# Performance work log

Hardware: AMD Instinct MI355X
Metric: run time of the kernel (lower is better)

Reference implementation:

```python
import jax, jax.numpy as jnp
import numpy as np

N = 100000          # total nodes
G = 128             # number of graphs
D_IN, D_H, D_OUT = 512, 1024, 512
E = 1600000         # edges (unused by the math, matches forward signature)


def setup_inputs() -> dict:
    key = jax.random.key(0)
    ks = jax.random.split(key, 9)
    x = jax.random.normal(ks[0], (N, D_IN), dtype=jnp.float32)
    edge_index = jax.random.randint(ks[1], (2, E), 0, N, dtype=jnp.int64)
    # sorted batch ids; guarantee every graph id appears at least once
    batch = jnp.sort(jnp.concatenate([
        jnp.arange(G, dtype=jnp.int64),
        jax.random.randint(ks[2], (N - G,), 0, G, dtype=jnp.int64),
    ]))
    s = 0.02
    W0 = jax.random.normal(ks[3], (D_IN, D_H), dtype=jnp.float32) * s
    b0 = jnp.zeros((D_H,), dtype=jnp.float32)
    W1 = jax.random.normal(ks[4], (D_H, D_H), dtype=jnp.float32) * s
    b1 = jnp.zeros((D_H,), dtype=jnp.float32)
    W2 = jax.random.normal(ks[5], (D_H, D_OUT), dtype=jnp.float32) * s
    b2 = jnp.zeros((D_OUT,), dtype=jnp.float32)
    return {"x": x, "edge_index": edge_index, "batch": batch,
            "W0": W0, "b0": b0, "W1": W1, "b1": b1, "W2": W2, "b2": b2}


def reference(x, edge_index, batch, W0, b0, W1, b1, W2, b2):
    # Linear + ReLU stack (dropout p=0 -> identity in eval). edge_index is unused,
    # matching the original module (its 'GCN' layer is a plain nn.Linear).
    h = jax.nn.relu(x @ W0 + b0)
    h = jax.nn.relu(h @ W1 + b1)
    h = jax.nn.relu(h @ W2 + b2)        # [N, D_OUT]
    # global mean pool per graph: fused segment-sum replaces the per-graph mask loop
    sums = jax.ops.segment_sum(h, batch, num_segments=G)                 # [G, D_OUT]
    counts = jax.ops.segment_sum(jnp.ones((h.shape[0],), h.dtype), batch,
                                 num_segments=G)                          # [G]
    return sums / counts[:, None]
```

## Files before the change

kernel.cpp:

```cpp
#include <hip/hip_runtime.h>
#include <cstdint>
#include <cstddef>

typedef __bf16 bf16x8 __attribute__((ext_vector_type(8)));
typedef float f32x4 __attribute__((ext_vector_type(4)));

__device__ __forceinline__ unsigned short f2bf(float f) {
  unsigned u = __float_as_uint(f);
  u += 0x7fffu + ((u >> 16) & 1u);
  return (unsigned short)(u >> 16);
}
__device__ __forceinline__ float bf2f(unsigned short s) {
  return __uint_as_float(((unsigned)s) << 16);
}

__device__ __forceinline__ void gld_lds16(const void* g, void* l) {
  __builtin_amdgcn_global_load_lds(
      (const __attribute__((address_space(1))) void*)g,
      (__attribute__((address_space(3))) void*)l, 16, 0, 0);
}

#define BARM() do { __builtin_amdgcn_s_barrier(); asm volatile("" ::: "memory"); } while (0)
#define VMCNT(n) asm volatile("s_waitcnt vmcnt(" #n ")" ::: "memory")
#define LGKM0()  do { asm volatile("s_waitcnt lgkmcnt(0)" ::: "memory"); \
                      __builtin_amdgcn_sched_barrier(0); } while (0)

__global__ void transpose_w(const float* __restrict__ w, unsigned short* __restrict__ wt,
                            int K, int N) {
  __shared__ float tile[32][33];
  int nt = N >> 5;
  int bx = blockIdx.x % nt;
  int by = blockIdx.x / nt;
  int tx = threadIdx.x & 31, ty = threadIdx.x >> 5;
#pragma unroll
  for (int r = 0; r < 32; r += 8)
    tile[ty + r][tx] = w[(size_t)(by * 32 + ty + r) * N + bx * 32 + tx];
  __syncthreads();
#pragma unroll
  for (int r = 0; r < 32; r += 8)
    wt[(size_t)(bx * 32 + ty + r) * K + by * 32 + tx] = f2bf(tile[tx][ty + r]);
}

__global__ void cvt_x(const float* __restrict__ x, unsigned short* __restrict__ xb,
                      int rows, int nvalid, int D) {
  size_t total = (size_t)rows * D / 8;
  for (size_t i = (size_t)blockIdx.x * blockDim.x + threadIdx.x; i < total;
       i += (size_t)gridDim.x * blockDim.x) {
    size_t e = i * 8;
    int row = (int)(e / (size_t)D);
    uint4 ov;
    if (row < nvalid) {
      const float4* s = (const float4*)(x + e);
      float4 v0 = s[0], v1 = s[1];
      ov.x = (unsigned)f2bf(v0.x) | ((unsigned)f2bf(v0.y) << 16);
      ov.y = (unsigned)f2bf(v0.z) | ((unsigned)f2bf(v0.w) << 16);
      ov.z = (unsigned)f2bf(v1.x) | ((unsigned)f2bf(v1.y) << 16);
      ov.w = (unsigned)f2bf(v1.z) | ((unsigned)f2bf(v1.w) << 16);
    } else {
      ov.x = ov.y = ov.z = ov.w = 0u;
    }
    *(uint4*)(xb + e) = ov;
  }
}

__device__ __forceinline__ bf16x8 read_frag(const unsigned short* region, int row, int kel) {
  int ke = kel ^ (((row >> 1) & 3) << 3);
  return *(const bf16x8*)(region + row * 32 + ke);
}

template <int R>
__device__ __forceinline__ void stage_rows(const unsigned short* gpanel, int K, int kofs,
                                           unsigned short* region, int tid) {
#pragma unroll
  for (int r = 0; r < R / 64; ++r) {
    int row = r * 64 + (tid >> 2);
    int ke = ((tid & 3) * 8) ^ (((row >> 1) & 3) << 3);
    gld_lds16(gpanel + (size_t)row * K + kofs + ke, region + r * 2048 + tid * 8);
  }
}

__global__ __launch_bounds__(256, 2) void gemm256x128(
    const unsigned short* __restrict__ A,
    const unsigned short* __restrict__ Bt,
    const float* __restrict__ bias,
    unsigned short* __restrict__ C,
    int N, int K) {
  __shared__ alignas(16) unsigned short lds[2][12288];
  const int tid = threadIdx.x;
  const int w = tid >> 6, l = tid & 63;
  const int wm = w >> 1, wn = w & 1;
  const int lc = l & 15, lk8 = (l >> 4) * 8;

  const int nbn = N >> 7;
  const int nwg = gridDim.x;
  const int q = nwg >> 3, rr = nwg & 7;
  const int xcd = blockIdx.x & 7, ib = blockIdx.x >> 3;
  const int bswz = (xcd < rr ? xcd * (q + 1) : rr * (q + 1) + (xcd - rr) * q) + ib;
  const int bm = bswz / nbn, bn = bswz - bm * nbn;

  const unsigned short* Ap = A + (size_t)bm * 256 * K;
  const unsigned short* Bp = Bt + (size_t)bn * 128 * K;
  const int T = K >> 5;

  f32x4 acc[8][4] = {};

  stage_rows<256>(Ap, K, 0, &lds[0][0], tid);
  stage_rows<128>(Bp, K, 0, &lds[0][8192], tid);
  VMCNT(0);
  BARM();

  for (int t = 0; t < T; ++t) {
    const int s = t & 1;
    const unsigned short* As = &lds[s][0];
    const unsigned short* Bs = &lds[s][8192];
    bf16x8 a[8], b[4];

#pragma unroll
    for (int mm = 0; mm < 8; ++mm) a[mm] = read_frag(As, wm * 128 + mm * 16 + lc, lk8);
#pragma unroll
    for (int nn = 0; nn < 4; ++nn) b[nn] = read_frag(Bs, wn * 64 + nn * 16 + lc, lk8);
    if (t + 1 < T) {
      stage_rows<256>(Ap, K, (t + 1) * 32, &lds[s ^ 1][0], tid);
      stage_rows<128>(Bp, K, (t + 1) * 32, &lds[s ^ 1][8192], tid);
    }
    BARM();
    LGKM0();
    __builtin_amdgcn_s_setprio(1);
#pragma unroll
    for (int mm = 0; mm < 8; ++mm)
#pragma unroll
      for (int nn = 0; nn < 4; ++nn)
        acc[mm][nn] = __builtin_amdgcn_mfma_f32_16x16x32_bf16(a[mm], b[nn], acc[mm][nn], 0, 0, 0);
    __builtin_amdgcn_s_setprio(0);
    VMCNT(0);
    BARM();
  }

  unsigned short* eps = &lds[0][0];
  float bv[4];
#pragma unroll
  for (int nn = 0; nn < 4; ++nn) bv[nn] = bias[bn * 128 + wn * 64 + nn * 16 + lc];

#pragma unroll
  for (int r = 0; r < 2; ++r) {
    if (wm == r) {
#pragma unroll
      for (int mm = 0; mm < 8; ++mm) {
#pragma unroll
        for (int nn = 0; nn < 4; ++nn) {
          int lcol = wn * 64 + nn * 16 + lc;
#pragma unroll
          for (int j = 0; j < 4; ++j) {
            int lrow = mm * 16 + (l >> 4) * 4 + j;
            int g = lcol >> 3, e = lcol & 7;
            float v = fmaxf(acc[mm][nn][j] + bv[nn], 0.0f);
            eps[lrow * 128 + ((g ^ (lrow & 15)) << 3) + e] = f2bf(v);
          }
        }
      }
    }
    BARM();
#pragma unroll
    for (int it = 0; it < 8; ++it) {
      int flat = it * 256 + tid;
      int lrow = flat >> 4, cb = flat & 15;
      uint4 v = *(const uint4*)&eps[lrow * 128 + (((cb ^ (lrow & 15))) << 3)];
      *(uint4*)&C[(size_t)(bm * 256 + r * 128 + lrow) * N + bn * 128 + cb * 8] = v;
    }
    BARM();
  }
}

__global__ void pool_partial(const unsigned short* __restrict__ h2, const int* __restrict__ batch,
                             float* __restrict__ part, int n, int D, int S) {
  int g = blockIdx.x / S, sub = blockIdx.x - g * S;
  int lo, hi;
  { int a = 0, b = n; while (a < b) { int m = (a + b) >> 1; if (batch[m] < g) a = m + 1; else b = m; } lo = a; }
  { int a = lo, b = n; while (a < b) { int m = (a + b) >> 1; if (batch[m] < g + 1) a = m + 1; else b = m; } hi = a; }
  int t = threadIdx.x;
  float sx = 0.f, sy = 0.f;
  for (int r = lo + sub; r < hi; r += S) {
    unsigned v = *(const unsigned*)(h2 + (size_t)r * D + t * 2);
    sx += bf2f((unsigned short)(v & 0xffffu));
    sy += bf2f((unsigned short)(v >> 16));
  }
  float* o = part + (size_t)blockIdx.x * D + t * 2;
  o[0] = sx;
  o[1] = sy;
}

__global__ void pool_reduce(const float* __restrict__ part, const int* __restrict__ batch,
                            float* __restrict__ out, int n, int D, int S, int G) {
  int idx = blockIdx.x * blockDim.x + threadIdx.x;
  if (idx >= G * D) return;
  int g = idx / D, d = idx - g * D;
  int lo, hi;
  { int a = 0, b = n; while (a < b) { int m = (a + b) >> 1; if (batch[m] < g) a = m + 1; else b = m; } lo = a; }
  { int a = lo, b = n; while (a < b) { int m = (a + b) >> 1; if (batch[m] < g + 1) a = m + 1; else b = m; } hi = a; }
  float sum = 0.f;
  for (int k = 0; k < S; ++k) sum += part[(size_t)(g * S + k) * D + d];
  out[idx] = sum / (float)(hi - lo);
}

static inline size_t align256(size_t x) { return (x + 255) & ~(size_t)255; }

extern "C" void kernel_launch(void* const* d_in, const int* in_sizes, int n_in,
                              void* d_out, int out_size, void* d_ws, size_t ws_size,
                              hipStream_t stream) {
  const float* x = (const float*)d_in[0];
  const int* batch = (const int*)d_in[2];
  const float* W0 = (const float*)d_in[3];
  const float* b0 = (const float*)d_in[4];
  const float* W1 = (const float*)d_in[5];
  const float* b1 = (const float*)d_in[6];
  const float* W2 = (const float*)d_in[7];
  const float* b2 = (const float*)d_in[8];
  float* out = (float*)d_out;

  const int Nn = in_sizes[2];
  const int DIN = 512, DH = 1024, DOUT = 512;
  const int G = out_size / DOUT;
  const int S = 8;
  const int Mpad = ((Nn + 255) / 256) * 256;

  uint8_t* p = (uint8_t*)d_ws;
  unsigned short* W0t = (unsigned short*)p; p += align256((size_t)DH * DIN * 2);
  unsigned short* W1t = (unsigned short*)p; p += align256((size_t)DH * DH * 2);
  unsigned short* W2t = (unsigned short*)p; p += align256((size_t)DOUT * DH * 2);
  unsigned short* h2  = (unsigned short*)p; p += align256((size_t)Mpad * DOUT * 2);
  float* part         = (float*)p;          p += align256((size_t)G * S * DOUT * 4);
  size_t used = (size_t)(p - (uint8_t*)d_ws);
  size_t avail = ws_size > used ? ws_size - used : 0;
  size_t per_row = (size_t)(DIN + DH + DH) * 2;
  long long chl = (long long)(avail / per_row);
  chl = (chl / 256) * 256;
  int CH = (int)(chl < 256 ? 256 : chl);
  if (CH > Mpad) CH = Mpad;
  unsigned short* xb = (unsigned short*)p; p += align256((size_t)CH * DIN * 2);
  unsigned short* h0 = (unsigned short*)p; p += align256((size_t)CH * DH * 2);
  unsigned short* h1 = (unsigned short*)p; p += align256((size_t)CH * DH * 2);

  transpose_w<<<dim3((DIN / 32) * (DH / 32)), 256, 0, stream>>>(W0, W0t, DIN, DH);
  transpose_w<<<dim3((DH / 32) * (DH / 32)), 256, 0, stream>>>(W1, W1t, DH, DH);
  transpose_w<<<dim3((DH / 32) * (DOUT / 32)), 256, 0, stream>>>(W2, W2t, DH, DOUT);

  for (int off = 0; off < Mpad; off += CH) {
    int rows = Mpad - off; if (rows > CH) rows = CH;
    int nvalid = Nn - off;
    size_t cvt_threads = (size_t)rows * DIN / 8;
    int cvt_blocks = (int)((cvt_threads + 255) / 256);
    if (cvt_blocks > 2048) cvt_blocks = 2048;
    cvt_x<<<dim3(cvt_blocks), 256, 0, stream>>>(x + (size_t)off * DIN, xb, rows, nvalid, DIN);

    gemm256x128<<<dim3((rows / 256) * (DH / 128)), 256, 0, stream>>>(xb, W0t, b0, h0, DH, DIN);
    gemm256x128<<<dim3((rows / 256) * (DH / 128)), 256, 0, stream>>>(h0, W1t, b1, h1, DH, DH);
    gemm256x128<<<dim3((rows / 256) * (DOUT / 128)), 256, 0, stream>>>(
        h1, W2t, b2, h2 + (size_t)off * DOUT, DOUT, DH);
  }

  pool_partial<<<dim3(G * S), 256, 0, stream>>>(h2, batch, part, Nn, DOUT, S);
  pool_reduce<<<dim3((G * DOUT + 255) / 256), 256, 0, stream>>>(part, batch, out, Nn, DOUT, S, G);
}
```

Baseline: 739.8 us.

## Pre-pack weights into MFMA fragment order and load B directly to registers

```diff
diff --git a/kernel.cpp b/kernel.cpp
--- a/kernel.cpp
+++ b/kernel.cpp
@@ -25,20 +25,27 @@
 #define LGKM0()  do { asm volatile("s_waitcnt lgkmcnt(0)" ::: "memory"); \
                       __builtin_amdgcn_sched_barrier(0); } while (0)
 
-__global__ void transpose_w(const float* __restrict__ w, unsigned short* __restrict__ wt,
-                            int K, int N) {
+__global__ void pack_w(const float* __restrict__ w, unsigned short* __restrict__ wp,
+                       int K, int N) {
   __shared__ float tile[32][33];
-  int nt = N >> 5;
-  int bx = blockIdx.x % nt;
-  int by = blockIdx.x / nt;
+  int nt32 = N >> 5;
+  int bx = blockIdx.x % nt32;
+  int by = blockIdx.x / nt32;
   int tx = threadIdx.x & 31, ty = threadIdx.x >> 5;
 #pragma unroll
   for (int r = 0; r < 32; r += 8)
     tile[ty + r][tx] = w[(size_t)(by * 32 + ty + r) * N + bx * 32 + tx];
   __syncthreads();
-#pragma unroll
-  for (int r = 0; r < 32; r += 8)
-    wt[(size_t)(bx * 32 + ty + r) * K + by * 32 + tx] = f2bf(tile[tx][ty + r]);
+  int KQ = K >> 5;
+  int flat = threadIdx.x * 4;
+  int c = flat >> 9;
+  int l = (flat >> 3) & 63;
+  int e0 = flat & 7;
+  int nl = c * 16 + (l & 15);
+  int kl = (l >> 4) * 8 + e0;
+  unsigned short* o = wp + ((size_t)((bx * 2 + c) * KQ + by) * 64 + l) * 8 + e0;
+#pragma unroll
+  for (int e = 0; e < 4; ++e) o[e] = f2bf(tile[kl + e][nl]);
 }
 
 __global__ void cvt_x(const float* __restrict__ x, unsigned short* __restrict__ xb,
@@ -68,24 +75,30 @@
   return *(const bf16x8*)(region + row * 32 + ke);
 }
 
-template <int R>
-__device__ __forceinline__ void stage_rows(const unsigned short* gpanel, int K, int kofs,
-                                           unsigned short* region, int tid) {
-#pragma unroll
-  for (int r = 0; r < R / 64; ++r) {
+__device__ __forceinline__ void stage_a(const unsigned short* gpanel, int K, int kofs,
+                                        unsigned short* region, int tid) {
+#pragma unroll
+  for (int r = 0; r < 4; ++r) {
     int row = r * 64 + (tid >> 2);
     int ke = ((tid & 3) * 8) ^ (((row >> 1) & 3) << 3);
     gld_lds16(gpanel + (size_t)row * K + kofs + ke, region + r * 2048 + tid * 8);
   }
 }
 
-__global__ __launch_bounds__(256, 2) void gemm256x128(
+__device__ __forceinline__ void load_b4(const unsigned short* wpb, int KQ, int kq, int l,
+                                        bf16x8* b) {
+#pragma unroll
+  for (int nn = 0; nn < 4; ++nn)
+    b[nn] = *(const bf16x8*)(wpb + ((size_t)(nn * KQ + kq) * 64 + l) * 8);
+}
+
+__global__ __launch_bounds__(256, 2) void gemm_blds(
     const unsigned short* __restrict__ A,
-    const unsigned short* __restrict__ Bt,
+    const unsigned short* __restrict__ Wp,
     const float* __restrict__ bias,
     unsigned short* __restrict__ C,
     int N, int K) {
-  __shared__ alignas(16) unsigned short lds[2][12288];
+  __shared__ alignas(16) unsigned short lds[2][8192];
   const int tid = threadIdx.x;
   const int w = tid >> 6, l = tid & 63;
   const int wm = w >> 1, wn = w & 1;
@@ -99,42 +112,44 @@
   const int bm = bswz / nbn, bn = bswz - bm * nbn;
 
   const unsigned short* Ap = A + (size_t)bm * 256 * K;
-  const unsigned short* Bp = Bt + (size_t)bn * 128 * K;
-  const int T = K >> 5;
+  const int KQ = K >> 5;
+  const unsigned short* wpb = Wp + ((size_t)(bn * 8 + wn * 4) * KQ * 64) * 8;
+  const int T = KQ;
 
   f32x4 acc[8][4] = {};
-
-  stage_rows<256>(Ap, K, 0, &lds[0][0], tid);
-  stage_rows<128>(Bp, K, 0, &lds[0][8192], tid);
+  bf16x8 a[8], bc[4], bn_[4];
+
+  stage_a(Ap, K, 0, &lds[0][0], tid);
+  load_b4(wpb, KQ, 0, l, bc);
   VMCNT(0);
   BARM();
 
-  for (int t = 0; t < T; ++t) {
-    const int s = t & 1;
-    const unsigned short* As = &lds[s][0];
-    const unsigned short* Bs = &lds[s][8192];
-    bf16x8 a[8], b[4];
-
-#pragma unroll
-    for (int mm = 0; mm < 8; ++mm) a[mm] = read_frag(As, wm * 128 + mm * 16 + lc, lk8);
-#pragma unroll
-    for (int nn = 0; nn < 4; ++nn) b[nn] = read_frag(Bs, wn * 64 + nn * 16 + lc, lk8);
-    if (t + 1 < T) {
-      stage_rows<256>(Ap, K, (t + 1) * 32, &lds[s ^ 1][0], tid);
-      stage_rows<128>(Bp, K, (t + 1) * 32, &lds[s ^ 1][8192], tid);
-    }
-    BARM();
-    LGKM0();
-    __builtin_amdgcn_s_setprio(1);
-#pragma unroll
-    for (int mm = 0; mm < 8; ++mm)
-#pragma unroll
-      for (int nn = 0; nn < 4; ++nn)
-        acc[mm][nn] = __builtin_amdgcn_mfma_f32_16x16x32_bf16(a[mm], b[nn], acc[mm][nn], 0, 0, 0);
-    __builtin_amdgcn_s_setprio(0);
-    VMCNT(0);
-    BARM();
-  }
+#define TILE_BODY(TT, SRD, SWR, BCUR, BNXT)                                      \
+  do {                                                                           \
+    _Pragma("unroll") for (int mm = 0; mm < 8; ++mm)                             \
+        a[mm] = read_frag(SRD, wm * 128 + mm * 16 + lc, lk8);                    \
+    if ((TT) + 1 < T) {                                                          \
+      stage_a(Ap, K, ((TT) + 1) * 32, SWR, tid);                                 \
+      load_b4(wpb, KQ, (TT) + 1, l, BNXT);                                       \
+    }                                                                            \
+    BARM();                                                                      \
+    LGKM0();                                                                     \
+    __builtin_amdgcn_s_setprio(1);                                               \
+    _Pragma("unroll") for (int mm = 0; mm < 8; ++mm)                             \
+        _Pragma("unroll") for (int nn = 0; nn < 4; ++nn)                         \
+            acc[mm][nn] = __builtin_amdgcn_mfma_f32_16x16x32_bf16(               \
+                a[mm], BCUR[nn], acc[mm][nn], 0, 0, 0);                          \
+    __builtin_amdgcn_s_setprio(0);                                               \
+    VMCNT(0);                                                                    \
+    BARM();                                                                      \
+  } while (0)
+
+  for (int t = 0; t < T; t += 2) {
+    TILE_BODY(t, &lds[0][0], &lds[1][0], bc, bn_);
+    if (t + 1 < T)
+      TILE_BODY(t + 1, &lds[1][0], &lds[0][0], bn_, bc);
+  }
+#undef TILE_BODY
 
   unsigned short* eps = &lds[0][0];
   float bv[4];
@@ -224,9 +239,9 @@
   const int Mpad = ((Nn + 255) / 256) * 256;
 
   uint8_t* p = (uint8_t*)d_ws;
-  unsigned short* W0t = (unsigned short*)p; p += align256((size_t)DH * DIN * 2);
-  unsigned short* W1t = (unsigned short*)p; p += align256((size_t)DH * DH * 2);
-  unsigned short* W2t = (unsigned short*)p; p += align256((size_t)DOUT * DH * 2);
+  unsigned short* W0p = (unsigned short*)p; p += align256((size_t)DH * DIN * 2);
+  unsigned short* W1p = (unsigned short*)p; p += align256((size_t)DH * DH * 2);
+  unsigned short* W2p = (unsigned short*)p; p += align256((size_t)DOUT * DH * 2);
   unsigned short* h2  = (unsigned short*)p; p += align256((size_t)Mpad * DOUT * 2);
   float* part         = (float*)p;          p += align256((size_t)G * S * DOUT * 4);
   size_t used = (size_t)(p - (uint8_t*)d_ws);
@@ -240,9 +255,9 @@
   unsigned short* h0 = (unsigned short*)p; p += align256((size_t)CH * DH * 2);
   unsigned short* h1 = (unsigned short*)p; p += align256((size_t)CH * DH * 2);
 
-  transpose_w<<<dim3((DIN / 32) * (DH / 32)), 256, 0, stream>>>(W0, W0t, DIN, DH);
-  transpose_w<<<dim3((DH / 32) * (DH / 32)), 256, 0, stream>>>(W1, W1t, DH, DH);
-  transpose_w<<<dim3((DH / 32) * (DOUT / 32)), 256, 0, stream>>>(W2, W2t, DH, DOUT);
+  pack_w<<<dim3((DH / 32) * (DIN / 32)), 256, 0, stream>>>(W0, W0p, DIN, DH);
+  pack_w<<<dim3((DH / 32) * (DH / 32)), 256, 0, stream>>>(W1, W1p, DH, DH);
+  pack_w<<<dim3((DOUT / 32) * (DH / 32)), 256, 0, stream>>>(W2, W2p, DH, DOUT);
 
   for (int off = 0; off < Mpad; off += CH) {
     int rows = Mpad - off; if (rows > CH) rows = CH;
@@ -252,10 +267,10 @@
     if (cvt_blocks > 2048) cvt_blocks = 2048;
     cvt_x<<<dim3(cvt_blocks), 256, 0, stream>>>(x + (size_t)off * DIN, xb, rows, nvalid, DIN);
 
-    gemm256x128<<<dim3((rows / 256) * (DH / 128)), 256, 0, stream>>>(xb, W0t, b0, h0, DH, DIN);
-    gemm256x128<<<dim3((rows / 256) * (DH / 128)), 256, 0, stream>>>(h0, W1t, b1, h1, DH, DH);
-    gemm256x128<<<dim3((rows / 256) * (DOUT / 128)), 256, 0, stream>>>(
-        h1, W2t, b2, h2 + (size_t)off * DOUT, DOUT, DH);
+    gemm_blds<<<dim3((rows / 256) * (DH / 128)), 256, 0, stream>>>(xb, W0p, b0, h0, DH, DIN);
+    gemm_blds<<<dim3((rows / 256) * (DH / 128)), 256, 0, stream>>>(h0, W1p, b1, h1, DH, DH);
+    gemm_blds<<<dim3((rows / 256) * (DOUT / 128)), 256, 0, stream>>>(
+        h1, W2p, b2, h2 + (size_t)off * DOUT, DOUT, DH);
   }
 
   pool_partial<<<dim3(G * S), 256, 0, stream>>>(h2, batch, part, Nn, DOUT, S);
```

Measured after the change: 756.4 us. +2.2%, slower.
